# Kernel tuning notes

Hardware: AMD Instinct MI355X
Metric: run time of the kernel (lower is better)

Reference implementation:

```python
import jax, jax.numpy as jnp
import numpy as np

IN_DIM = 512

def setup_inputs() -> dict:
    key = jax.random.key(0)
    ks = jax.random.split(key, 7)
    s = 1.0 / np.sqrt(IN_DIM)
    x = jax.random.normal(ks[0], (8, 2048, IN_DIM), dtype=jnp.float32)
    Wq = jax.random.uniform(ks[1], (IN_DIM, IN_DIM), jnp.float32, -s, s)
    bq = jax.random.uniform(ks[2], (IN_DIM,), jnp.float32, -s, s)
    Wk = jax.random.uniform(ks[3], (IN_DIM, IN_DIM), jnp.float32, -s, s)
    bk = jax.random.uniform(ks[4], (IN_DIM,), jnp.float32, -s, s)
    Wv = jax.random.uniform(ks[5], (IN_DIM, IN_DIM), jnp.float32, -s, s)
    bv = jax.random.uniform(ks[6], (IN_DIM,), jnp.float32, -s, s)
    return {"x": x, "Wq": Wq, "bq": bq, "Wk": Wk, "bk": bk, "Wv": Wv, "bv": bv}

def reference(x, Wq, bq, Wk, bk, Wv, bv):
    # Q,K,V projections: torch Linear is x @ W.T + b; Wq here is [out,in]
    q = jnp.einsum('bsc,dc->bsd', x, Wq) + bq
    k = jnp.einsum('bsc,dc->bsd', x, Wk) + bk
    v = jnp.einsum('bsc,dc->bsd', x, Wv) + bv
    energy = jnp.einsum('bqd,bkd->bqk', q, k)  # no scaling, matches source
    attention = jax.nn.softmax(energy, axis=-1)
    out = jnp.einsum('bqk,bkd->bqd', attention, v)
    return out
```

## Files before the change

kernel.cpp:

```cpp
#include <hip/hip_runtime.h>

typedef unsigned short u16;
typedef _Float16 f16;

using half8   = __attribute__((ext_vector_type(8))) _Float16;
using f32x4   = __attribute__((ext_vector_type(4))) float;
using ushort8 = __attribute__((ext_vector_type(8))) unsigned short;
using us4     = __attribute__((ext_vector_type(4))) unsigned short;
using float4v = __attribute__((ext_vector_type(4))) float;

#define B_  8
#define S_  2048
#define D_  512
#define BK  32
#define TILE_ELEMS 4096
#define BUF_ELEMS  8192

__device__ __forceinline__ u16 f2h(float f) {
  f16 h = (f16)f;
  u16 u;
  __builtin_memcpy(&u, &h, 2);
  return u;
}

__device__ __forceinline__ float h2f(u16 h) {
  f16 x;
  __builtin_memcpy(&x, &h, 2);
  return (float)x;
}

__device__ __forceinline__ void stage16(const void* g, void* l) {
  __builtin_amdgcn_global_load_lds((const __attribute__((address_space(1))) void*)g,
                                   (__attribute__((address_space(3))) void*)l,
                                   16, 0, 0);
}

__device__ __forceinline__ void xcd_remap(int& bx, int& by, int& bz) {
  const int lin = ((int)blockIdx.z * (int)gridDim.y + (int)blockIdx.y) * (int)gridDim.x
                  + (int)blockIdx.x;
  const int nwg = (int)gridDim.x * (int)gridDim.y * (int)gridDim.z;
  const int swz = (lin & 7) * (nwg >> 3) + (lin >> 3);
  bx = swz % (int)gridDim.x;
  const int tmp = swz / (int)gridDim.x;
  by = tmp % (int)gridDim.y;
  bz = tmp / (int)gridDim.y;
}

__device__ __forceinline__ void gemm_core(const u16* __restrict__ A, const u16* __restrict__ B,
                                          int K, int m0, int n0,
                                          u16* lds, f32x4 acc[4][4]) {
  const int tid  = threadIdx.x;
  const int lane = tid & 63;
  const int wave = tid >> 6;
  const int wr = wave >> 1, wc = wave & 1;
  const int fr   = lane & 15;
  const int fgrp = lane >> 4;

  int sr[2], sc[2];
  #pragma unroll
  for (int s = 0; s < 2; ++s) {
    const int p    = tid * 16 + s * 4096;
    const int R    = p >> 7;
    const int slot = (p >> 4) & 7;
    const int s0   = slot ^ (R & 7);
    sr[s] = 2 * R + (s0 >> 2);
    sc[s] = (s0 & 3) * 8;
  }

  int offA[4], offB[4];
  #pragma unroll
  for (int m = 0; m < 4; ++m) {
    const int ra = wr * 64 + m * 16 + fr;
    const int Ra = ra >> 1;
    offA[m] = Ra * 128 + (((((ra & 1) << 2) | fgrp) ^ (Ra & 7)) << 4);
    const int rb = wc * 64 + m * 16 + fr;
    const int Rb = rb >> 1;
    offB[m] = Rb * 128 + (((((rb & 1) << 2) | fgrp) ^ (Rb & 7)) << 4);
  }

  const f32x4 vzero = {0.f, 0.f, 0.f, 0.f};
  #pragma unroll
  for (int m = 0; m < 4; ++m)
    #pragma unroll
    for (int n = 0; n < 4; ++n)
      acc[m][n] = vzero;

  const int T = K / BK;

  auto STAGE = [&](int t, u16* buf) {
    #pragma unroll
    for (int s = 0; s < 2; ++s) {
      stage16(A + (size_t)(m0 + sr[s]) * K + t * BK + sc[s],
              buf + s * 2048 + wave * 512);
      stage16(B + (size_t)(n0 + sr[s]) * K + t * BK + sc[s],
              buf + TILE_ELEMS + s * 2048 + wave * 512);
    }
  };

  STAGE(0, lds);
  STAGE(1, lds + BUF_ELEMS);
  STAGE(2, lds + 2 * BUF_ELEMS);

  int t = 0;
#define GEMM_ITER(WN)                                                            \
  {                                                                              \
    asm volatile("s_waitcnt vmcnt(" #WN ")\n\ts_barrier" ::: "memory");          \
    const u16* buf = lds + (t & 3) * BUF_ELEMS;                                  \
    half8 a[4], b[4];                                                            \
    _Pragma("unroll")                                                            \
    for (int m = 0; m < 4; ++m)                                                  \
      a[m] = *(const half8*)((const char*)buf + offA[m]);                        \
    _Pragma("unroll")                                                            \
    for (int n = 0; n < 4; ++n)                                                  \
      b[n] = *(const half8*)((const char*)(buf + TILE_ELEMS) + offB[n]);         \
    if (t + 3 < T) STAGE(t + 3, lds + ((t + 3) & 3) * BUF_ELEMS);                \
    __builtin_amdgcn_s_setprio(1);                                               \
    _Pragma("unroll")                                                            \
    for (int m = 0; m < 4; ++m)                                                  \
      _Pragma("unroll")                                                          \
      for (int n = 0; n < 4; ++n)                                                \
        acc[m][n] = __builtin_amdgcn_mfma_f32_16x16x32_f16(a[m], b[n],           \
                                                           acc[m][n], 0, 0, 0); \
    __builtin_amdgcn_s_setprio(0);                                               \
  }

  for (; t < T - 2; ++t) GEMM_ITER(8)
  GEMM_ITER(4); ++t;
  GEMM_ITER(0);
#undef GEMM_ITER
}

__global__ __launch_bounds__(256) void proj_kernel(
    const u16* __restrict__ xh, const u16* __restrict__ Wh,
    const float* __restrict__ bq, const float* __restrict__ bk, const float* __restrict__ bv,
    u16* __restrict__ Qb, u16* __restrict__ Kb, u16* __restrict__ Vt) {
  __shared__ __align__(16) u16 lds[4 * BUF_ELEMS];
  int bx, by, bz;
  xcd_remap(bx, by, bz);
  const int z  = bz;
  const int m0 = by * 128;
  const int n0 = bx * 128;
  const u16* W = Wh + (size_t)z * D_ * D_;
  const float* bias = (z == 0) ? bq : (z == 1) ? bk : bv;
  f32x4 acc[4][4];
  gemm_core(xh, W, D_, m0, n0, lds, acc);

  const int lane = threadIdx.x & 63;
  const int wave = threadIdx.x >> 6;
  const int wr = wave >> 1, wc = wave & 1;
  #pragma unroll
  for (int m = 0; m < 4; ++m) {
    const int gr0 = m0 + wr * 64 + m * 16 + ((lane >> 4) << 2);
    #pragma unroll
    for (int n = 0; n < 4; ++n) {
      const int gc = n0 + wc * 64 + n * 16 + (lane & 15);
      const float bb = bias[gc];
      if (z < 2) {
        u16* O = z ? Kb : Qb;
        #pragma unroll
        for (int r = 0; r < 4; ++r)
          O[(size_t)(gr0 + r) * D_ + gc] = f2h(acc[m][n][r] + bb);
      } else {
        const int bidx = gr0 >> 11;
        const int s    = gr0 & 2047;
        us4 p;
        #pragma unroll
        for (int r = 0; r < 4; ++r) p[r] = f2h(acc[m][n][r] + bb);
        *(us4*)(Vt + ((size_t)bidx * D_ + gc) * S_ + s) = p;
      }
    }
  }
}

__global__ __launch_bounds__(256) void qk_kernel(
    const u16* __restrict__ Qb, const u16* __restrict__ Kb, u16* __restrict__ E,
    size_t sA, size_t sE) {
  __shared__ __align__(16) u16 lds[4 * BUF_ELEMS];
  int bx, by, bz;
  xcd_remap(bx, by, bz);
  const int z  = bz;
  const int m0 = by * 128;
  const int n0 = bx * 128;
  f32x4 acc[4][4];
  gemm_core(Qb + (size_t)z * sA, Kb + (size_t)z * sA, D_, m0, n0, lds, acc);

  u16* Eb = E + (size_t)z * sE;
  const int lane = threadIdx.x & 63;
  const int wave = threadIdx.x >> 6;
  const int wr = wave >> 1, wc = wave & 1;
  #pragma unroll
  for (int m = 0; m < 4; ++m) {
    const int gr0 = m0 + wr * 64 + m * 16 + ((lane >> 4) << 2);
    #pragma unroll
    for (int n = 0; n < 4; ++n) {
      const int gc = n0 + wc * 64 + n * 16 + (lane & 15);
      #pragma unroll
      for (int r = 0; r < 4; ++r)
        Eb[(size_t)(gr0 + r) * S_ + gc] = f2h(acc[m][n][r]);
    }
  }
}

__global__ __launch_bounds__(256) void softmax_kernel(u16* __restrict__ E) {
  const int row  = blockIdx.x * 4 + (threadIdx.x >> 6);
  const int lane = threadIdx.x & 63;
  u16* R = E + (size_t)row * S_;
  float e[32];
  #pragma unroll
  for (int i = 0; i < 4; ++i) {
    ushort8 v = *(const ushort8*)(R + i * 512 + lane * 8);
    #pragma unroll
    for (int j = 0; j < 8; ++j) e[i * 8 + j] = h2f(v[j]);
  }
  float m = e[0];
  #pragma unroll
  for (int i = 1; i < 32; ++i) m = fmaxf(m, e[i]);
  for (int off = 32; off > 0; off >>= 1) m = fmaxf(m, __shfl_xor(m, off, 64));
  float s = 0.f;
  #pragma unroll
  for (int i = 0; i < 32; ++i) { e[i] = __expf(e[i] - m); s += e[i]; }
  for (int off = 32; off > 0; off >>= 1) s += __shfl_xor(s, off, 64);
  const float inv = 1.f / s;
  #pragma unroll
  for (int i = 0; i < 4; ++i) {
    ushort8 v;
    #pragma unroll
    for (int j = 0; j < 8; ++j) v[j] = f2h(e[i * 8 + j] * inv);
    *(ushort8*)(R + i * 512 + lane * 8) = v;
  }
}

__global__ __launch_bounds__(256) void pv_kernel(
    const u16* __restrict__ P, const u16* __restrict__ Vt, float* __restrict__ out,
    size_t sP, size_t sV, size_t sO) {
  __shared__ __align__(16) u16 lds[4 * BUF_ELEMS];
  int bx, by, bz;
  xcd_remap(bx, by, bz);
  const int z  = bz;
  const int m0 = by * 128;
  const int n0 = bx * 128;
  f32x4 acc[4][4];
  gemm_core(P + (size_t)z * sP, Vt + (size_t)z * sV, S_, m0, n0, lds, acc);

  float* Ob = out + (size_t)z * sO;
  const int lane = threadIdx.x & 63;
  const int wave = threadIdx.x >> 6;
  const int wr = wave >> 1, wc = wave & 1;
  #pragma unroll
  for (int m = 0; m < 4; ++m) {
    const int gr0 = m0 + wr * 64 + m * 16 + ((lane >> 4) << 2);
    #pragma unroll
    for (int n = 0; n < 4; ++n) {
      const int gc = n0 + wc * 64 + n * 16 + (lane & 15);
      #pragma unroll
      for (int r = 0; r < 4; ++r)
        Ob[(size_t)(gr0 + r) * D_ + gc] = acc[m][n][r];
    }
  }
}

__global__ __launch_bounds__(256) void cvt_kernel(const float* __restrict__ in,
                                                  u16* __restrict__ out, int n8) {
  const int i = blockIdx.x * 256 + threadIdx.x;
  if (i >= n8) return;
  const float4v a = *(const float4v*)(in + (size_t)i * 8);
  const float4v b = *(const float4v*)(in + (size_t)i * 8 + 4);
  ushort8 o;
  o[0] = f2h(a[0]); o[1] = f2h(a[1]); o[2] = f2h(a[2]); o[3] = f2h(a[3]);
  o[4] = f2h(b[0]); o[5] = f2h(b[1]); o[6] = f2h(b[2]); o[7] = f2h(b[3]);
  *(ushort8*)(out + (size_t)i * 8) = o;
}

__global__ __launch_bounds__(256) void cvt3_kernel(const float* __restrict__ w0,
                                                   const float* __restrict__ w1,
                                                   const float* __restrict__ w2,
                                                   u16* __restrict__ out, int n8) {
  const int i = blockIdx.x * 256 + threadIdx.x;
  if (i >= n8) return;
  const float* in = (blockIdx.y == 0) ? w0 : (blockIdx.y == 1) ? w1 : w2;
  u16* o_ = out + (size_t)blockIdx.y * D_ * D_;
  const float4v a = *(const float4v*)(in + (size_t)i * 8);
  const float4v b = *(const float4v*)(in + (size_t)i * 8 + 4);
  ushort8 o;
  o[0] = f2h(a[0]); o[1] = f2h(a[1]); o[2] = f2h(a[2]); o[3] = f2h(a[3]);
  o[4] = f2h(b[0]); o[5] = f2h(b[1]); o[6] = f2h(b[2]); o[7] = f2h(b[3]);
  *(ushort8*)(o_ + (size_t)i * 8) = o;
}

extern "C" void kernel_launch(void* const* d_in, const int* in_sizes, int n_in,
                              void* d_out, int out_size, void* d_ws, size_t ws_size,
                              hipStream_t stream) {
  (void)in_sizes; (void)n_in; (void)out_size;
  const float* x  = (const float*)d_in[0];
  const float* Wq = (const float*)d_in[1];
  const float* bq = (const float*)d_in[2];
  const float* Wk = (const float*)d_in[3];
  const float* bk = (const float*)d_in[4];
  const float* Wv = (const float*)d_in[5];
  const float* bv = (const float*)d_in[6];
  float* out = (float*)d_out;

  char* ws = (char*)d_ws;
  size_t off = 0;
  auto alloc = [&](size_t bytes) -> char* {
    char* p = ws + off;
    off += (bytes + 255) & ~(size_t)255;
    return p;
  };
  const size_t MS = (size_t)B_ * S_;
  u16* xh = (u16*)alloc(MS * D_ * 2);
  u16* Wh = (u16*)alloc(3ull * D_ * D_ * 2);
  u16* Qb = (u16*)alloc(MS * D_ * 2);
  u16* Kb = (u16*)alloc(MS * D_ * 2);
  u16* Vt = (u16*)alloc(MS * D_ * 2);
  const size_t Efull = (size_t)B_ * S_ * S_ * 2;
  const bool full = ws_size >= off + Efull;
  u16* E = (u16*)alloc(full ? Efull : (size_t)S_ * S_ * 2);

  {
    const int n8 = (int)(MS * D_ / 8);
    cvt_kernel<<<dim3((n8 + 255) / 256), dim3(256), 0, stream>>>(x, xh, n8);
    const int w8 = D_ * D_ / 8;
    cvt3_kernel<<<dim3((w8 + 255) / 256, 3), dim3(256), 0, stream>>>(Wq, Wk, Wv, Wh, w8);
  }

  proj_kernel<<<dim3(D_ / 128, MS / 128, 3), dim3(256), 0, stream>>>(
      xh, Wh, bq, bk, bv, Qb, Kb, Vt);

  if (full) {
    qk_kernel<<<dim3(S_ / 128, S_ / 128, B_), dim3(256), 0, stream>>>(
        Qb, Kb, E, (size_t)S_ * D_, (size_t)S_ * S_);
    softmax_kernel<<<dim3(B_ * S_ / 4), dim3(256), 0, stream>>>(E);
    pv_kernel<<<dim3(D_ / 128, S_ / 128, B_), dim3(256), 0, stream>>>(
        E, Vt, out, (size_t)S_ * S_, (size_t)D_ * S_, (size_t)S_ * D_);
  } else {
    for (int b = 0; b < B_; ++b) {
      qk_kernel<<<dim3(S_ / 128, S_ / 128, 1), dim3(256), 0, stream>>>(
          Qb + (size_t)b * S_ * D_, Kb + (size_t)b * S_ * D_, E, 0, 0);
      softmax_kernel<<<dim3(S_ / 4), dim3(256), 0, stream>>>(E);
      pv_kernel<<<dim3(D_ / 128, S_ / 128, 1), dim3(256), 0, stream>>>(
          E, Vt + (size_t)b * D_ * S_, out + (size_t)b * S_ * D_, 0, 0, 0);
    }
  }
}
```

Baseline: 160.6 us.

## Enlarge GEMM tiles to 256x256 with 8-wave blocks for all matmuls

Generalizes the shared GEMM core into a template that uses 512-thread blocks (2x4 waves) and 256-wide N tiles, with 256-row M tiles for the projection and QK kernels and 128-row tiles for PV. Larger tiles raise arithmetic intensity and cut global/L2 traffic per FLOP for the operand loads. In exchange, LDS use grows to 128 KB per block for proj/qk, accumulator registers double, occupancy drops, and the grids get fewer blocks (QK goes to 512 blocks, proj to 384), which may underfill the GPU.

```diff
diff --git a/kernel.cpp b/kernel.cpp
--- a/kernel.cpp
+++ b/kernel.cpp
@@ -13,8 +13,6 @@
 #define S_  2048
 #define D_  512
 #define BK  32
-#define TILE_ELEMS 4096
-#define BUF_ELEMS  8192
 
 __device__ __forceinline__ u16 f2h(float f) {
   f16 h = (f16)f;
@@ -46,41 +44,51 @@
   bz = tmp / (int)gridDim.y;
 }
 
-__device__ __forceinline__ void gemm_core(const u16* __restrict__ A, const u16* __restrict__ B,
-                                          int K, int m0, int n0,
-                                          u16* lds, f32x4 acc[4][4]) {
+template<int M_REP>
+__device__ __forceinline__ void gemm_core256(const u16* __restrict__ A,
+                                             const u16* __restrict__ B,
+                                             int K, int m0, int n0,
+                                             u16* lds, f32x4 acc[M_REP][4]) {
+  constexpr int BM      = M_REP * 32;
+  constexpr int A_ELEMS = BM * 32;
+  constexpr int BUFE    = (BM + 256) * 32;
+  constexpr int SA      = BM / 128;
+
   const int tid  = threadIdx.x;
   const int lane = tid & 63;
   const int wave = tid >> 6;
-  const int wr = wave >> 1, wc = wave & 1;
+  const int wr = wave >> 2, wc = wave & 3;
   const int fr   = lane & 15;
   const int fgrp = lane >> 4;
 
-  int sr[2], sc[2];
+  int sra[2], sca[2], srb[2], scb[2];
   #pragma unroll
   for (int s = 0; s < 2; ++s) {
-    const int p    = tid * 16 + s * 4096;
+    const int p    = tid * 16 + s * 8192;
     const int R    = p >> 7;
     const int slot = (p >> 4) & 7;
     const int s0   = slot ^ (R & 7);
-    sr[s] = 2 * R + (s0 >> 2);
-    sc[s] = (s0 & 3) * 8;
-  }
-
-  int offA[4], offB[4];
-  #pragma unroll
-  for (int m = 0; m < 4; ++m) {
-    const int ra = wr * 64 + m * 16 + fr;
+    sra[s] = srb[s] = 2 * R + (s0 >> 2);
+    sca[s] = scb[s] = (s0 & 3) * 8;
+  }
+
+  int offA[M_REP], offB[4];
+  #pragma unroll
+  for (int m = 0; m < M_REP; ++m) {
+    const int ra = wr * (M_REP * 16) + m * 16 + fr;
     const int Ra = ra >> 1;
     offA[m] = Ra * 128 + (((((ra & 1) << 2) | fgrp) ^ (Ra & 7)) << 4);
-    const int rb = wc * 64 + m * 16 + fr;
+  }
+  #pragma unroll
+  for (int n = 0; n < 4; ++n) {
+    const int rb = wc * 64 + n * 16 + fr;
     const int Rb = rb >> 1;
-    offB[m] = Rb * 128 + (((((rb & 1) << 2) | fgrp) ^ (Rb & 7)) << 4);
+    offB[n] = Rb * 128 + (((((rb & 1) << 2) | fgrp) ^ (Rb & 7)) << 4);
   }
 
   const f32x4 vzero = {0.f, 0.f, 0.f, 0.f};
   #pragma unroll
-  for (int m = 0; m < 4; ++m)
+  for (int m = 0; m < M_REP; ++m)
     #pragma unroll
     for (int n = 0; n < 4; ++n)
       acc[m][n] = vzero;
@@ -89,34 +97,35 @@
 
   auto STAGE = [&](int t, u16* buf) {
     #pragma unroll
-    for (int s = 0; s < 2; ++s) {
-      stage16(A + (size_t)(m0 + sr[s]) * K + t * BK + sc[s],
-              buf + s * 2048 + wave * 512);
-      stage16(B + (size_t)(n0 + sr[s]) * K + t * BK + sc[s],
-              buf + TILE_ELEMS + s * 2048 + wave * 512);
-    }
+    for (int s = 0; s < SA; ++s)
+      stage16(A + (size_t)(m0 + sra[s]) * K + t * BK + sca[s],
+              buf + s * 4096 + wave * 512);
+    #pragma unroll
+    for (int s = 0; s < 2; ++s)
+      stage16(B + (size_t)(n0 + srb[s]) * K + t * BK + scb[s],
+              buf + A_ELEMS + s * 4096 + wave * 512);
   };
 
   STAGE(0, lds);
-  STAGE(1, lds + BUF_ELEMS);
-  STAGE(2, lds + 2 * BUF_ELEMS);
+  STAGE(1, lds + BUFE);
+  STAGE(2, lds + 2 * BUFE);
 
   int t = 0;
 #define GEMM_ITER(WN)                                                            \
   {                                                                              \
     asm volatile("s_waitcnt vmcnt(" #WN ")\n\ts_barrier" ::: "memory");          \
-    const u16* buf = lds + (t & 3) * BUF_ELEMS;                                  \
-    half8 a[4], b[4];                                                            \
+    const u16* buf = lds + (t & 3) * BUFE;                                       \
+    half8 a[M_REP], b[4];                                                        \
     _Pragma("unroll")                                                            \
-    for (int m = 0; m < 4; ++m)                                                  \
+    for (int m = 0; m < M_REP; ++m)                                              \
       a[m] = *(const half8*)((const char*)buf + offA[m]);                        \
     _Pragma("unroll")                                                            \
     for (int n = 0; n < 4; ++n)                                                  \
-      b[n] = *(const half8*)((const char*)(buf + TILE_ELEMS) + offB[n]);         \
-    if (t + 3 < T) STAGE(t + 3, lds + ((t + 3) & 3) * BUF_ELEMS);                \
+      b[n] = *(const half8*)((const char*)(buf + A_ELEMS) + offB[n]);            \
+    if (t + 3 < T) STAGE(t + 3, lds + ((t + 3) & 3) * BUFE);                     \
     __builtin_amdgcn_s_setprio(1);                                               \
     _Pragma("unroll")                                                            \
-    for (int m = 0; m < 4; ++m)                                                  \
+    for (int m = 0; m < M_REP; ++m)                                              \
       _Pragma("unroll")                                                          \
       for (int n = 0; n < 4; ++n)                                                \
         acc[m][n] = __builtin_amdgcn_mfma_f32_16x16x32_f16(a[m], b[n],           \
@@ -124,33 +133,39 @@
     __builtin_amdgcn_s_setprio(0);                                               \
   }
 
-  for (; t < T - 2; ++t) GEMM_ITER(8)
-  GEMM_ITER(4); ++t;
-  GEMM_ITER(0);
+  if constexpr (SA == 2) {
+    for (; t < T - 2; ++t) GEMM_ITER(8)
+    GEMM_ITER(4); ++t;
+    GEMM_ITER(0);
+  } else {
+    for (; t < T - 2; ++t) GEMM_ITER(6)
+    GEMM_ITER(3); ++t;
+    GEMM_ITER(0);
+  }
 #undef GEMM_ITER
 }
 
-__global__ __launch_bounds__(256) void proj_kernel(
+__global__ __launch_bounds__(512) void proj_kernel(
     const u16* __restrict__ xh, const u16* __restrict__ Wh,
     const float* __restrict__ bq, const float* __restrict__ bk, const float* __restrict__ bv,
     u16* __restrict__ Qb, u16* __restrict__ Kb, u16* __restrict__ Vt) {
-  __shared__ __align__(16) u16 lds[4 * BUF_ELEMS];
+  __shared__ __align__(16) u16 lds[4 * (256 + 256) * 32];
   int bx, by, bz;
   xcd_remap(bx, by, bz);
   const int z  = bz;
-  const int m0 = by * 128;
-  const int n0 = bx * 128;
+  const int m0 = by * 256;
+  const int n0 = bx * 256;
   const u16* W = Wh + (size_t)z * D_ * D_;
   const float* bias = (z == 0) ? bq : (z == 1) ? bk : bv;
-  f32x4 acc[4][4];
-  gemm_core(xh, W, D_, m0, n0, lds, acc);
+  f32x4 acc[8][4];
+  gemm_core256<8>(xh, W, D_, m0, n0, lds, acc);
 
   const int lane = threadIdx.x & 63;
   const int wave = threadIdx.x >> 6;
-  const int wr = wave >> 1, wc = wave & 1;
-  #pragma unroll
-  for (int m = 0; m < 4; ++m) {
-    const int gr0 = m0 + wr * 64 + m * 16 + ((lane >> 4) << 2);
+  const int wr = wave >> 2, wc = wave & 3;
+  #pragma unroll
+  for (int m = 0; m < 8; ++m) {
+    const int gr0 = m0 + wr * 128 + m * 16 + ((lane >> 4) << 2);
     #pragma unroll
     for (int n = 0; n < 4; ++n) {
       const int gc = n0 + wc * 64 + n * 16 + (lane & 15);
@@ -172,25 +187,25 @@
   }
 }
 
-__global__ __launch_bounds__(256) void qk_kernel(
+__global__ __launch_bounds__(512) void qk_kernel(
     const u16* __restrict__ Qb, const u16* __restrict__ Kb, u16* __restrict__ E,
     size_t sA, size_t sE) {
-  __shared__ __align__(16) u16 lds[4 * BUF_ELEMS];
+  __shared__ __align__(16) u16 lds[4 * (256 + 256) * 32];
   int bx, by, bz;
   xcd_remap(bx, by, bz);
   const int z  = bz;
-  const int m0 = by * 128;
-  const int n0 = bx * 128;
-  f32x4 acc[4][4];
-  gemm_core(Qb + (size_t)z * sA, Kb + (size_t)z * sA, D_, m0, n0, lds, acc);
+  const int m0 = by * 256;
+  const int n0 = bx * 256;
+  f32x4 acc[8][4];
+  gemm_core256<8>(Qb + (size_t)z * sA, Kb + (size_t)z * sA, D_, m0, n0, lds, acc);
 
   u16* Eb = E + (size_t)z * sE;
   const int lane = threadIdx.x & 63;
   const int wave = threadIdx.x >> 6;
-  const int wr = wave >> 1, wc = wave & 1;
-  #pragma unroll
-  for (int m = 0; m < 4; ++m) {
-    const int gr0 = m0 + wr * 64 + m * 16 + ((lane >> 4) << 2);
+  const int wr = wave >> 2, wc = wave & 3;
+  #pragma unroll
+  for (int m = 0; m < 8; ++m) {
+    const int gr0 = m0 + wr * 128 + m * 16 + ((lane >> 4) << 2);
     #pragma unroll
     for (int n = 0; n < 4; ++n) {
       const int gc = n0 + wc * 64 + n * 16 + (lane & 15);
@@ -230,22 +245,22 @@
   }
 }
 
-__global__ __launch_bounds__(256) void pv_kernel(
+__global__ __launch_bounds__(512) void pv_kernel(
     const u16* __restrict__ P, const u16* __restrict__ Vt, float* __restrict__ out,
     size_t sP, size_t sV, size_t sO) {
-  __shared__ __align__(16) u16 lds[4 * BUF_ELEMS];
+  __shared__ __align__(16) u16 lds[4 * (128 + 256) * 32];
   int bx, by, bz;
   xcd_remap(bx, by, bz);
   const int z  = bz;
   const int m0 = by * 128;
-  const int n0 = bx * 128;
+  const int n0 = bx * 256;
   f32x4 acc[4][4];
-  gemm_core(P + (size_t)z * sP, Vt + (size_t)z * sV, S_, m0, n0, lds, acc);
+  gemm_core256<4>(P + (size_t)z * sP, Vt + (size_t)z * sV, S_, m0, n0, lds, acc);
 
   float* Ob = out + (size_t)z * sO;
   const int lane = threadIdx.x & 63;
   const int wave = threadIdx.x >> 6;
-  const int wr = wave >> 1, wc = wave & 1;
+  const int wr = wave >> 2, wc = wave & 3;
   #pragma unroll
   for (int m = 0; m < 4; ++m) {
     const int gr0 = m0 + wr * 64 + m * 16 + ((lane >> 4) << 2);
@@ -324,21 +339,21 @@
     cvt3_kernel<<<dim3((w8 + 255) / 256, 3), dim3(256), 0, stream>>>(Wq, Wk, Wv, Wh, w8);
   }
 
-  proj_kernel<<<dim3(D_ / 128, MS / 128, 3), dim3(256), 0, stream>>>(
+  proj_kernel<<<dim3(D_ / 256, MS / 256, 3), dim3(512), 0, stream>>>(
       xh, Wh, bq, bk, bv, Qb, Kb, Vt);
 
   if (full) {
-    qk_kernel<<<dim3(S_ / 128, S_ / 128, B_), dim3(256), 0, stream>>>(
+    qk_kernel<<<dim3(S_ / 256, S_ / 256, B_), dim3(512), 0, stream>>>(
         Qb, Kb, E, (size_t)S_ * D_, (size_t)S_ * S_);
     softmax_kernel<<<dim3(B_ * S_ / 4), dim3(256), 0, stream>>>(E);
-    pv_kernel<<<dim3(D_ / 128, S_ / 128, B_), dim3(256), 0, stream>>>(
+    pv_kernel<<<dim3(D_ / 256, S_ / 128, B_), dim3(512), 0, stream>>>(
         E, Vt, out, (size_t)S_ * S_, (size_t)D_ * S_, (size_t)S_ * D_);
   } else {
     for (int b = 0; b < B_; ++b) {
-      qk_kernel<<<dim3(S_ / 128, S_ / 128, 1), dim3(256), 0, stream>>>(
+      qk_kernel<<<dim3(S_ / 256, S_ / 256, 1), dim3(512), 0, stream>>>(
           Qb + (size_t)b * S_ * D_, Kb + (size_t)b * S_ * D_, E, 0, 0);
       softmax_kernel<<<dim3(S_ / 4), dim3(256), 0, stream>>>(E);
-      pv_kernel<<<dim3(D_ / 128, S_ / 128, 1), dim3(256), 0, stream>>>(
+      pv_kernel<<<dim3(D_ / 256, S_ / 128, 1), dim3(512), 0, stream>>>(
           E, Vt + (size_t)b * D_ * S_, out + (size_t)b * S_ * D_, 0, 0, 0);
     }
   }
```

Result: slower. 164.6 us (+2.4%).
